# Performance work log

Measured on AMD Instinct MI355X. Metric: run time of the kernel, lower is better.

## Reference

```python
import jax, jax.numpy as jnp
import numpy as np

T, D_IN, H, KV, HD = 1024, 2048, 32, 8, 64
GROUP = H // KV  # 4
EPS = 1e-6


def _rmsnorm(x, w):
    inv_rms = jax.lax.rsqrt(jnp.mean(x * x, axis=-1, keepdims=True) + EPS)
    return x * inv_rms * w


def _rope(x, cos, sin):
    # x: [heads, T, HD]; cos/sin: [T, HD]
    hd = x.shape[-1]
    x1, x2 = x[..., : hd // 2], x[..., hd // 2 :]
    rotated = jnp.concatenate([-x2, x1], axis=-1)
    return x * cos[None, :, :] + rotated * sin[None, :, :]


def setup_inputs() -> dict:
    key = jax.random.key(0)
    ks = jax.random.split(key, 6)
    x = jax.random.normal(ks[0], (T, D_IN), dtype=jnp.float32)
    # RoPE tables (cos/sin over [T, HD])
    inv_freq = 1.0 / (10000.0 ** (np.arange(0, HD, 2, dtype=np.float64) / HD))
    ang = np.arange(T, dtype=np.float64)[:, None] * inv_freq[None, :]
    emb = np.concatenate([ang, ang], axis=-1)
    cos = jnp.asarray(np.cos(emb), dtype=jnp.float32)
    sin = jnp.asarray(np.sin(emb), dtype=jnp.float32)
    # causal mask: True above diagonal -> masked to -inf
    mask = jnp.triu(jnp.ones((T, T), dtype=jnp.bool_), k=1)
    # kaiming_normal fan_in (relu): std = sqrt(2/fan_in)
    Wq = jax.random.normal(ks[1], (H * HD, D_IN), jnp.float32) * (2.0 / D_IN) ** 0.5
    Wk = jax.random.normal(ks[2], (KV * HD, D_IN), jnp.float32) * (2.0 / D_IN) ** 0.5
    Wv = jax.random.normal(ks[3], (KV * HD, D_IN), jnp.float32) * (2.0 / D_IN) ** 0.5
    Wo = jax.random.normal(ks[4], (D_IN, H * HD), jnp.float32) * (2.0 / (H * HD)) ** 0.5
    q_norm_w = jnp.ones((HD,), jnp.float32)
    k_norm_w = jnp.ones((HD,), jnp.float32)
    one = jnp.ones((1,), jnp.float32)
    return {
        "x": x, "scale_x": one, "mask": mask,
        "cos": cos, "scale_cos": one, "sin": sin, "scale_sin": one,
        "Wq": Wq, "Wk": Wk, "Wv": Wv, "Wo": Wo,
        "q_norm_w": q_norm_w, "k_norm_w": k_norm_w,
    }


def reference(x, scale_x, mask, cos, scale_cos, sin, scale_sin,
              Wq, Wk, Wv, Wo, q_norm_w, k_norm_w):
    num_tokens = x.shape[0]
    # QKV projections
    q = (x @ Wq.T).reshape(num_tokens, H, HD).transpose(1, 0, 2)   # [H, T, HD]
    k = (x @ Wk.T).reshape(num_tokens, KV, HD).transpose(1, 0, 2)  # [KV, T, HD]
    v = (x @ Wv.T).reshape(num_tokens, KV, HD).transpose(1, 0, 2)  # [KV, T, HD]
    # qk_norm
    q = _rmsnorm(q, q_norm_w)
    k = _rmsnorm(k, k_norm_w)
    # RoPE
    q = _rope(q, cos, sin)
    k = _rope(k, cos, sin)
    # expand KV groups to all heads (repeat_interleave along head axis)
    k = jnp.repeat(k, GROUP, axis=0)  # [H, T, HD]
    v = jnp.repeat(v, GROUP, axis=0)  # [H, T, HD]
    # attention scores
    qk = jnp.einsum("htd,hsd->hts", q, k) / (HD ** 0.5)
    qk = jnp.where(mask[None, :, :], -jnp.inf, qk)
    attn = jax.nn.softmax(qk, axis=-1)
    out = jnp.einsum("hts,hsd->htd", attn, v)          # [H, T, HD]
    out = out.transpose(1, 0, 2).reshape(num_tokens, H * HD)
    return out @ Wo.T  # [T, D_IN]
```

## Files before the change

kernel.cpp:

```cpp
#include <hip/hip_runtime.h>

typedef __bf16 bf16x8 __attribute__((ext_vector_type(8)));
typedef float f32x4 __attribute__((ext_vector_type(4)));

#define T_TOK 1024
#define DIN   2048
#define NH    32
#define NKV   8
#define HD    64

__device__ __forceinline__ unsigned short f2bf(float f) {
  unsigned int u = __float_as_uint(f);
  unsigned int r = (u + 0x7fffu + ((u >> 16) & 1u)) >> 16;
  return (unsigned short)r;
}

__device__ __forceinline__ void glds16(const void* g, void* lds) {
  __builtin_amdgcn_global_load_lds(
      (const __attribute__((address_space(1))) void*)g,
      (__attribute__((address_space(3))) void*)lds, 16, 0, 0);
}

__global__ __launch_bounds__(256) void k_cvt_all(
    const float* __restrict__ x,  const float* __restrict__ wq,
    const float* __restrict__ wk, const float* __restrict__ wv,
    const float* __restrict__ wo, unsigned short* __restrict__ xb,
    unsigned short* __restrict__ wqkv, unsigned short* __restrict__ wob) {
  const long NX = 1l << 21, NWQ = 1l << 22, NWK = 1l << 20, NWV = 1l << 20;
  long i4 = ((long)blockIdx.x * blockDim.x + threadIdx.x) * 4;
  const float* src;
  unsigned short* dst;
  long off;
  if (i4 < NX)                       { src = x;  dst = xb;   off = i4; }
  else if (i4 < NX + NWQ)            { src = wq; dst = wqkv; off = i4 - NX; }
  else if (i4 < NX + NWQ + NWK)      { src = wk; dst = wqkv + NWQ; off = i4 - NX - NWQ; }
  else if (i4 < NX + NWQ + NWK + NWV){ src = wv; dst = wqkv + NWQ + NWK; off = i4 - NX - NWQ - NWK; }
  else                               { src = wo; dst = wob;  off = i4 - NX - NWQ - NWK - NWV; }
  float4 v = *reinterpret_cast<const float4*>(src + off);
  ushort4 o;
  o.x = f2bf(v.x); o.y = f2bf(v.y); o.z = f2bf(v.z); o.w = f2bf(v.w);
  *reinterpret_cast<ushort4*>(dst + off) = o;
}

template<int BN>
__global__ __launch_bounds__(256) void k_gemm2(
    const unsigned short* __restrict__ A, const unsigned short* __restrict__ B,
    float* __restrict__ C, int N, int K) {
  constexpr int NJ = BN / 32;
  constexpr int NBS = BN / 32;
  __shared__ unsigned short As[2][64 * 64];
  __shared__ unsigned short Bs[2][BN * 64];
  const int lane = threadIdx.x & 63;
  const int wave = threadIdx.x >> 6;
  const int wm = wave >> 1, wn = wave & 1;
  const int lr = lane & 15, lk = lane >> 4;
  const int brow = blockIdx.y * 64;
  const int bcol = blockIdx.x * BN;

  const int srow = lane >> 3;
  const int scol = ((lane & 7) ^ srow) * 8;
  const unsigned short* Ag = A + (long)(brow + srow) * K + scol;
  const unsigned short* Bg = B + (long)(bcol + srow) * K + scol;

  f32x4 acc[2][NJ];
#pragma unroll
  for (int i = 0; i < 2; i++)
#pragma unroll
    for (int j = 0; j < NJ; j++) acc[i][j] = (f32x4){0.f, 0.f, 0.f, 0.f};

  const int swz = (lr & 7) << 4;
  const int nt = K / 64;
  int cur = 0;

#pragma unroll
  for (int i = 0; i < 2; i++) {
    int strip = i * 4 + wave;
    glds16(Ag + (long)strip * 8 * K, (char*)As[0] + strip * 1024);
  }
#pragma unroll
  for (int i = 0; i < NBS; i++) {
    int strip = i * 4 + wave;
    glds16(Bg + (long)strip * 8 * K, (char*)Bs[0] + strip * 1024);
  }
  __syncthreads();

  for (int t = 0; t < nt; t++) {
    if (t + 1 < nt) {
      const int kk = (t + 1) * 64;
#pragma unroll
      for (int i = 0; i < 2; i++) {
        int strip = i * 4 + wave;
        glds16(Ag + (long)strip * 8 * K + kk, (char*)As[cur ^ 1] + strip * 1024);
      }
#pragma unroll
      for (int i = 0; i < NBS; i++) {
        int strip = i * 4 + wave;
        glds16(Bg + (long)strip * 8 * K + kk, (char*)Bs[cur ^ 1] + strip * 1024);
      }
    }
#pragma unroll
    for (int s = 0; s < 2; s++) {
      bf16x8 a[2], b[NJ];
#pragma unroll
      for (int i = 0; i < 2; i++) {
        int row = wm * 32 + i * 16 + lr;
        a[i] = *reinterpret_cast<const bf16x8*>(
            (const char*)As[cur] + row * 128 + ((s * 64 + lk * 16) ^ swz));
      }
#pragma unroll
      for (int j = 0; j < NJ; j++) {
        int row = wn * (BN / 2) + j * 16 + lr;
        b[j] = *reinterpret_cast<const bf16x8*>(
            (const char*)Bs[cur] + row * 128 + ((s * 64 + lk * 16) ^ swz));
      }
#pragma unroll
      for (int i = 0; i < 2; i++)
#pragma unroll
        for (int j = 0; j < NJ; j++)
          acc[i][j] = __builtin_amdgcn_mfma_f32_16x16x32_bf16(a[i], b[j], acc[i][j], 0, 0, 0);
    }
    __syncthreads();
    cur ^= 1;
  }

#pragma unroll
  for (int i = 0; i < 2; i++)
#pragma unroll
    for (int j = 0; j < NJ; j++)
#pragma unroll
      for (int p = 0; p < 4; p++)
        C[(long)(brow + wm * 32 + i * 16 + lk * 4 + p) * N +
          (bcol + wn * (BN / 2) + j * 16 + lr)] = acc[i][j][p];
}

__global__ void k_norm_rope(const float* __restrict__ qkv_lin,
                            unsigned short* __restrict__ qb, unsigned short* __restrict__ kb,
                            const float* __restrict__ cosT, const float* __restrict__ sinT,
                            const float* __restrict__ qw, const float* __restrict__ kw) {
  int gw = (blockIdx.x * blockDim.x + threadIdx.x) >> 6;
  int lane = threadIdx.x & 63;
  int t = gw / (NH + NKV);
  int hh = gw % (NH + NKV);
  if (t >= T_TOK) return;
  const float* base;
  unsigned short* ob;
  const float* w;
  if (hh < NH) {
    base = qkv_lin + (long)t * 3072 + hh * HD;
    ob   = qb + (long)t * (NH * HD) + hh * HD;
    w = qw;
  } else {
    int kh = hh - NH;
    base = qkv_lin + (long)t * 3072 + 2048 + kh * HD;
    ob   = kb + (long)t * (NKV * HD) + kh * HD;
    w = kw;
  }
  float v = base[lane];
  float ss = v * v;
#pragma unroll
  for (int off = 1; off < 64; off <<= 1) ss += __shfl_xor(ss, off);
  float xn = v * rsqrtf(ss * (1.0f / HD) + 1e-6f) * w[lane];
  float other = __shfl_xor(xn, 32);
  float c = cosT[t * HD + lane], s = sinT[t * HD + lane];
  ob[lane] = f2bf(xn * c + (lane < 32 ? -other : other) * s);
}

__global__ __launch_bounds__(256) void k_vt(const float* __restrict__ qkv_lin,
                                            unsigned short* __restrict__ out) {
  __shared__ float t[32][33];
  int tx = threadIdx.x & 31, ty = threadIdx.x >> 5;
  int r0 = blockIdx.y * 32;
  int c0 = blockIdx.x * 32;
#pragma unroll
  for (int r = 0; r < 4; r++)
    t[ty + r * 8][tx] = qkv_lin[(long)(r0 + ty + r * 8) * 3072 + 2560 + c0 + tx];
  __syncthreads();
#pragma unroll
  for (int r = 0; r < 4; r++)
    out[(long)(c0 + ty + r * 8) * 1024 + r0 + tx] = f2bf(t[tx][ty + r * 8]);
}

__global__ __launch_bounds__(64) void k_flash(
    const unsigned short* __restrict__ qb, const unsigned short* __restrict__ kb,
    const unsigned short* __restrict__ vtb, unsigned short* __restrict__ ao) {
  __shared__ unsigned short plds[16 * 64];
  const int rb = 63 - blockIdx.x;
  const int h  = blockIdx.y;
  const int kvh = h >> 2;
  const int lane = threadIdx.x & 63;
  const int lr = lane & 15, lk = lane >> 4;
  const int qrow = rb * 16;
  const int qt = rb >> 2;
  const int qrel = (rb & 3) * 16 + lr;
  const int pswz = (lr & 7) << 4;
  char* pbase = (char*)plds;
  const float SC = 0.125f * 1.44269504f;
  const f32x4 z4 = {0.f, 0.f, 0.f, 0.f};

  const unsigned short* qp = qb + (long)(qrow + lr) * (NH * HD) + h * HD + lk * 8;
  bf16x8 qa0 = *reinterpret_cast<const bf16x8*>(qp);
  bf16x8 qa1 = *reinterpret_cast<const bf16x8*>(qp + 32);

  f32x4 o[4];
#pragma unroll
  for (int f = 0; f < 4; f++) o[f] = z4;
  float m2 = -3.0e38f;
  float lp = 0.f;

  const int ntiles = qt + 1;
  for (int t = 0; t < ntiles; t++) {
    const unsigned short* kp = kb + (long)(t * 64 + lr) * 512 + kvh * 64 + lk * 8;
    bf16x8 kf0[4], kf1[4];
#pragma unroll
    for (int f = 0; f < 4; f++) {
      kf0[f] = *reinterpret_cast<const bf16x8*>(kp + (long)f * 16 * 512);
      kf1[f] = *reinterpret_cast<const bf16x8*>(kp + (long)f * 16 * 512 + 32);
    }
    const unsigned short* vp = vtb + (long)(kvh * 64 + lr) * 1024 + t * 64 + lk * 8;
    bf16x8 vfr[8];
#pragma unroll
    for (int fd = 0; fd < 4; fd++) {
      vfr[fd]     = *reinterpret_cast<const bf16x8*>(vp + (long)fd * 16 * 1024);
      vfr[4 + fd] = *reinterpret_cast<const bf16x8*>(vp + (long)fd * 16 * 1024 + 32);
    }
    f32x4 sacc[4];
    __builtin_amdgcn_s_setprio(1);
#pragma unroll
    for (int f = 0; f < 4; f++) {
      sacc[f] = __builtin_amdgcn_mfma_f32_16x16x32_bf16(kf0[f], qa0, z4, 0, 0, 0);
      sacc[f] = __builtin_amdgcn_mfma_f32_16x16x32_bf16(kf1[f], qa1, sacc[f], 0, 0, 0);
    }
    __builtin_amdgcn_s_setprio(0);
    const bool diag = (t == qt);
    float tmax = -3.0e38f;
#pragma unroll
    for (int f = 0; f < 4; f++)
#pragma unroll
      for (int p = 0; p < 4; p++) {
        float s_ = sacc[f][p] * SC;
        if (diag && (f * 16 + lk * 4 + p) > qrel) s_ = -3.0e38f;
        sacc[f][p] = s_;
        tmax = fmaxf(tmax, s_);
      }
    tmax = fmaxf(tmax, __shfl_xor(tmax, 16));
    tmax = fmaxf(tmax, __shfl_xor(tmax, 32));
    float mn = fmaxf(m2, tmax);
    float r = exp2f(m2 - mn);
    m2 = mn;
    float rp[4];
#pragma unroll
    for (int p = 0; p < 4; p++)
      rp[p] = __shfl(r, (lane & 48) | (lk * 4 + p));
    float ps = 0.f;
#pragma unroll
    for (int f = 0; f < 4; f++) {
      float e0 = exp2f(sacc[f][0] - mn), e1 = exp2f(sacc[f][1] - mn);
      float e2 = exp2f(sacc[f][2] - mn), e3 = exp2f(sacc[f][3] - mn);
      ps += (e0 + e1) + (e2 + e3);
      uint2 pk;
      pk.x = (unsigned)f2bf(e0) | ((unsigned)f2bf(e1) << 16);
      pk.y = (unsigned)f2bf(e2) | ((unsigned)f2bf(e3) << 16);
      *reinterpret_cast<uint2*>(pbase + lr * 128 + ((f * 32 + lk * 8) ^ pswz)) = pk;
    }
    lp = lp * r + ps;
#pragma unroll
    for (int fd = 0; fd < 4; fd++)
#pragma unroll
      for (int p = 0; p < 4; p++) o[fd][p] *= rp[p];
    __builtin_amdgcn_s_setprio(1);
#pragma unroll
    for (int ks = 0; ks < 2; ks++) {
      bf16x8 pa = *reinterpret_cast<const bf16x8*>(
          pbase + lr * 128 + ((ks * 64 + lk * 16) ^ pswz));
#pragma unroll
      for (int fd = 0; fd < 4; fd++)
        o[fd] = __builtin_amdgcn_mfma_f32_16x16x32_bf16(pa, vfr[ks * 4 + fd], o[fd], 0, 0, 0);
    }
    __builtin_amdgcn_s_setprio(0);
  }

  lp += __shfl_xor(lp, 16);
  lp += __shfl_xor(lp, 32);
  float lo[4];
#pragma unroll
  for (int p = 0; p < 4; p++) lo[p] = __shfl(lp, (lane & 48) | (lk * 4 + p));
#pragma unroll
  for (int fd = 0; fd < 4; fd++)
#pragma unroll
    for (int p = 0; p < 4; p++) {
      int qg = qrow + lk * 4 + p;
      int d = fd * 16 + lr;
      ao[(long)qg * (NH * HD) + h * HD + d] = f2bf(o[fd][p] / lo[p]);
    }
}

extern "C" void kernel_launch(void* const* d_in, const int* in_sizes, int n_in,
                              void* d_out, int out_size, void* d_ws, size_t ws_size,
                              hipStream_t stream) {
  const float* x    = (const float*)d_in[0];
  const float* cosT = (const float*)d_in[3];
  const float* sinT = (const float*)d_in[5];
  const float* Wq   = (const float*)d_in[7];
  const float* Wk   = (const float*)d_in[8];
  const float* Wv   = (const float*)d_in[9];
  const float* Wo   = (const float*)d_in[10];
  const float* qw   = (const float*)d_in[11];
  const float* kw   = (const float*)d_in[12];
  float* out = (float*)d_out;

  char* ws = (char*)d_ws;
  unsigned short* xb    = (unsigned short*)(ws);
  unsigned short* Wqkv  = (unsigned short*)(ws + (4u << 20));
  unsigned short* Wob   = (unsigned short*)(ws + (16u << 20));
  float* qkv_lin = (float*)(ws + (24u << 20));
  unsigned short* qbb = (unsigned short*)(ws + (36u << 20));
  unsigned short* kbb = (unsigned short*)(ws + (40u << 20));
  unsigned short* vtb = (unsigned short*)(ws + (41u << 20));
  unsigned short* ao  = (unsigned short*)(ws + (42u << 20));

  k_cvt_all<<<12288, 256, 0, stream>>>(x, Wq, Wk, Wv, Wo, xb, Wqkv, Wob);

  k_gemm2<64><<<dim3(48, 16), 256, 0, stream>>>(xb, Wqkv, qkv_lin, 3072, 2048);

  k_norm_rope<<<(T_TOK * (NH + NKV) * 64) / 256, 256, 0, stream>>>(
      qkv_lin, qbb, kbb, cosT, sinT, qw, kw);

  k_vt<<<dim3(16, 32), 256, 0, stream>>>(qkv_lin, vtb);

  k_flash<<<dim3(64, 32), 64, 0, stream>>>(qbb, kbb, vtb, ao);

  k_gemm2<64><<<dim3(32, 16), 256, 0, stream>>>(ao, Wob, out, 2048, 2048);
}
```

Measured before the change: 230.3 us.

## Share K/V tiles across GQA heads via LDS and enlarge GEMM tiles

The flash kernel now runs one 256-thread block per KV head and query block. Each of the four waves handles one query head of the group, and K and V^T tiles are staged in double-buffered LDS with async global-to-LDS loads. This removes the redundant per-head global reads of K/V and overlaps the next tile's load with compute. The GEMM is generalised to BMxBN tiles and both projections use 128x128 tiles, which increases operand reuse but leaves few blocks for the CU count.

```diff
diff --git a/kernel.cpp b/kernel.cpp
--- a/kernel.cpp
+++ b/kernel.cpp
@@ -42,19 +42,19 @@
   *reinterpret_cast<ushort4*>(dst + off) = o;
 }
 
-template<int BN>
+template<int BM, int BN>
 __global__ __launch_bounds__(256) void k_gemm2(
     const unsigned short* __restrict__ A, const unsigned short* __restrict__ B,
     float* __restrict__ C, int N, int K) {
+  constexpr int NI = BM / 32;
   constexpr int NJ = BN / 32;
-  constexpr int NBS = BN / 32;
-  __shared__ unsigned short As[2][64 * 64];
+  __shared__ unsigned short As[2][BM * 64];
   __shared__ unsigned short Bs[2][BN * 64];
   const int lane = threadIdx.x & 63;
   const int wave = threadIdx.x >> 6;
   const int wm = wave >> 1, wn = wave & 1;
   const int lr = lane & 15, lk = lane >> 4;
-  const int brow = blockIdx.y * 64;
+  const int brow = blockIdx.y * BM;
   const int bcol = blockIdx.x * BN;
 
   const int srow = lane >> 3;
@@ -62,9 +62,9 @@
   const unsigned short* Ag = A + (long)(brow + srow) * K + scol;
   const unsigned short* Bg = B + (long)(bcol + srow) * K + scol;
 
-  f32x4 acc[2][NJ];
-#pragma unroll
-  for (int i = 0; i < 2; i++)
+  f32x4 acc[NI][NJ];
+#pragma unroll
+  for (int i = 0; i < NI; i++)
 #pragma unroll
     for (int j = 0; j < NJ; j++) acc[i][j] = (f32x4){0.f, 0.f, 0.f, 0.f};
 
@@ -73,12 +73,12 @@
   int cur = 0;
 
 #pragma unroll
-  for (int i = 0; i < 2; i++) {
+  for (int i = 0; i < NI; i++) {
     int strip = i * 4 + wave;
     glds16(Ag + (long)strip * 8 * K, (char*)As[0] + strip * 1024);
   }
 #pragma unroll
-  for (int i = 0; i < NBS; i++) {
+  for (int i = 0; i < NJ; i++) {
     int strip = i * 4 + wave;
     glds16(Bg + (long)strip * 8 * K, (char*)Bs[0] + strip * 1024);
   }
@@ -88,22 +88,22 @@
     if (t + 1 < nt) {
       const int kk = (t + 1) * 64;
 #pragma unroll
-      for (int i = 0; i < 2; i++) {
+      for (int i = 0; i < NI; i++) {
         int strip = i * 4 + wave;
         glds16(Ag + (long)strip * 8 * K + kk, (char*)As[cur ^ 1] + strip * 1024);
       }
 #pragma unroll
-      for (int i = 0; i < NBS; i++) {
+      for (int i = 0; i < NJ; i++) {
         int strip = i * 4 + wave;
         glds16(Bg + (long)strip * 8 * K + kk, (char*)Bs[cur ^ 1] + strip * 1024);
       }
     }
 #pragma unroll
     for (int s = 0; s < 2; s++) {
-      bf16x8 a[2], b[NJ];
-#pragma unroll
-      for (int i = 0; i < 2; i++) {
-        int row = wm * 32 + i * 16 + lr;
+      bf16x8 a[NI], b[NJ];
+#pragma unroll
+      for (int i = 0; i < NI; i++) {
+        int row = wm * (BM / 2) + i * 16 + lr;
         a[i] = *reinterpret_cast<const bf16x8*>(
             (const char*)As[cur] + row * 128 + ((s * 64 + lk * 16) ^ swz));
       }
@@ -114,7 +114,7 @@
             (const char*)Bs[cur] + row * 128 + ((s * 64 + lk * 16) ^ swz));
       }
 #pragma unroll
-      for (int i = 0; i < 2; i++)
+      for (int i = 0; i < NI; i++)
 #pragma unroll
         for (int j = 0; j < NJ; j++)
           acc[i][j] = __builtin_amdgcn_mfma_f32_16x16x32_bf16(a[i], b[j], acc[i][j], 0, 0, 0);
@@ -124,12 +124,12 @@
   }
 
 #pragma unroll
-  for (int i = 0; i < 2; i++)
+  for (int i = 0; i < NI; i++)
 #pragma unroll
     for (int j = 0; j < NJ; j++)
 #pragma unroll
       for (int p = 0; p < 4; p++)
-        C[(long)(brow + wm * 32 + i * 16 + lk * 4 + p) * N +
+        C[(long)(brow + wm * (BM / 2) + i * 16 + lk * 4 + p) * N +
           (bcol + wn * (BN / 2) + j * 16 + lr)] = acc[i][j][p];
 }
 
@@ -180,22 +180,38 @@
     out[(long)(c0 + ty + r * 8) * 1024 + r0 + tx] = f2bf(t[tx][ty + r * 8]);
 }
 
-__global__ __launch_bounds__(64) void k_flash(
+__global__ __launch_bounds__(256) void k_flash(
     const unsigned short* __restrict__ qb, const unsigned short* __restrict__ kb,
     const unsigned short* __restrict__ vtb, unsigned short* __restrict__ ao) {
-  __shared__ unsigned short plds[16 * 64];
+  __shared__ unsigned short Ks[2][64 * 64];
+  __shared__ unsigned short Vs[2][64 * 64];
+  __shared__ unsigned short plds[4][16 * 64];
   const int rb = 63 - blockIdx.x;
-  const int h  = blockIdx.y;
-  const int kvh = h >> 2;
+  const int kvh = blockIdx.y;
   const int lane = threadIdx.x & 63;
+  const int wave = threadIdx.x >> 6;
+  const int h = kvh * 4 + wave;
   const int lr = lane & 15, lk = lane >> 4;
   const int qrow = rb * 16;
   const int qt = rb >> 2;
   const int qrel = (rb & 3) * 16 + lr;
   const int pswz = (lr & 7) << 4;
-  char* pbase = (char*)plds;
+  char* pbase = (char*)plds[wave];
   const float SC = 0.125f * 1.44269504f;
   const f32x4 z4 = {0.f, 0.f, 0.f, 0.f};
+
+  const int srow = lane >> 3;
+  const int scol = ((lane & 7) ^ srow) * 8;
+
+#define STAGE(buf, tt) do {                                                    \
+    _Pragma("unroll") for (int s_ = 0; s_ < 2; s_++) {                         \
+      int strip = s_ * 4 + wave;                                               \
+      glds16(kb + (long)((tt) * 64 + strip * 8 + srow) * 512 + kvh * 64 + scol,\
+             (char*)Ks[buf] + strip * 1024);                                   \
+      glds16(vtb + (long)(kvh * 64 + strip * 8 + srow) * 1024 + (tt) * 64 + scol,\
+             (char*)Vs[buf] + strip * 1024);                                   \
+    }                                                                          \
+  } while (0)
 
   const unsigned short* qp = qb + (long)(qrow + lr) * (NH * HD) + h * HD + lk * 8;
   bf16x8 qa0 = *reinterpret_cast<const bf16x8*>(qp);
@@ -208,20 +224,18 @@
   float lp = 0.f;
 
   const int ntiles = qt + 1;
+  int cur = 0;
+  STAGE(0, 0);
+  __syncthreads();
+
   for (int t = 0; t < ntiles; t++) {
-    const unsigned short* kp = kb + (long)(t * 64 + lr) * 512 + kvh * 64 + lk * 8;
+    if (t + 1 < ntiles) STAGE(cur ^ 1, t + 1);
     bf16x8 kf0[4], kf1[4];
 #pragma unroll
     for (int f = 0; f < 4; f++) {
-      kf0[f] = *reinterpret_cast<const bf16x8*>(kp + (long)f * 16 * 512);
-      kf1[f] = *reinterpret_cast<const bf16x8*>(kp + (long)f * 16 * 512 + 32);
-    }
-    const unsigned short* vp = vtb + (long)(kvh * 64 + lr) * 1024 + t * 64 + lk * 8;
-    bf16x8 vfr[8];
-#pragma unroll
-    for (int fd = 0; fd < 4; fd++) {
-      vfr[fd]     = *reinterpret_cast<const bf16x8*>(vp + (long)fd * 16 * 1024);
-      vfr[4 + fd] = *reinterpret_cast<const bf16x8*>(vp + (long)fd * 16 * 1024 + 32);
+      const char* kbase = (const char*)Ks[cur] + (f * 16 + lr) * 128;
+      kf0[f] = *reinterpret_cast<const bf16x8*>(kbase + ((lk * 16) ^ pswz));
+      kf1[f] = *reinterpret_cast<const bf16x8*>(kbase + ((64 + lk * 16) ^ pswz));
     }
     f32x4 sacc[4];
     __builtin_amdgcn_s_setprio(1);
@@ -267,6 +281,13 @@
     for (int fd = 0; fd < 4; fd++)
 #pragma unroll
       for (int p = 0; p < 4; p++) o[fd][p] *= rp[p];
+    bf16x8 vfr[8];
+#pragma unroll
+    for (int fd = 0; fd < 4; fd++) {
+      const char* vbase = (const char*)Vs[cur] + (fd * 16 + lr) * 128;
+      vfr[fd]     = *reinterpret_cast<const bf16x8*>(vbase + ((lk * 16) ^ pswz));
+      vfr[4 + fd] = *reinterpret_cast<const bf16x8*>(vbase + ((64 + lk * 16) ^ pswz));
+    }
     __builtin_amdgcn_s_setprio(1);
 #pragma unroll
     for (int ks = 0; ks < 2; ks++) {
@@ -277,6 +298,8 @@
         o[fd] = __builtin_amdgcn_mfma_f32_16x16x32_bf16(pa, vfr[ks * 4 + fd], o[fd], 0, 0, 0);
     }
     __builtin_amdgcn_s_setprio(0);
+    __syncthreads();
+    cur ^= 1;
   }
 
   lp += __shfl_xor(lp, 16);
@@ -292,6 +315,7 @@
       int d = fd * 16 + lr;
       ao[(long)qg * (NH * HD) + h * HD + d] = f2bf(o[fd][p] / lo[p]);
     }
+#undef STAGE
 }
 
 extern "C" void kernel_launch(void* const* d_in, const int* in_sizes, int n_in,
@@ -320,14 +344,14 @@
 
   k_cvt_all<<<12288, 256, 0, stream>>>(x, Wq, Wk, Wv, Wo, xb, Wqkv, Wob);
 
-  k_gemm2<64><<<dim3(48, 16), 256, 0, stream>>>(xb, Wqkv, qkv_lin, 3072, 2048);
+  k_gemm2<128, 128><<<dim3(24, 8), 256, 0, stream>>>(xb, Wqkv, qkv_lin, 3072, 2048);
 
   k_norm_rope<<<(T_TOK * (NH + NKV) * 64) / 256, 256, 0, stream>>>(
       qkv_lin, qbb, kbb, cosT, sinT, qw, kw);
 
   k_vt<<<dim3(16, 32), 256, 0, stream>>>(qkv_lin, vtb);
 
-  k_flash<<<dim3(64, 32), 64, 0, stream>>>(qbb, kbb, vtb, ao);
-
-  k_gemm2<64><<<dim3(32, 16), 256, 0, stream>>>(ao, Wob, out, 2048, 2048);
-}
+  k_flash<<<dim3(64, 8), 256, 0, stream>>>(qbb, kbb, vtb, ao);
+
+  k_gemm2<128, 128><<<dim3(16, 8), 256, 0, stream>>>(ao, Wob, out, 2048, 2048);
+}
```

Result: faster. 220.7 us (-4.2%).
